# Kernel optimization log

Measured on AMD Instinct MI355X. Metric: run time of the kernel, lower is better.

The kernel has to match this reference:

```python
import jax, jax.numpy as jnp
import numpy as np

B, T, D = 64, 1024, 256   # batch, steps, obs dim
H, L, S = 512, 64, 4      # rnn hidden, latent dim, num_samples
LOG_2PI = float(np.log(2.0 * np.pi))


def setup_inputs() -> dict:
    key = jax.random.key(0)
    ks = jax.random.split(key, 6)
    return {
        "inputs": jax.random.normal(ks[0], (B, T, D), dtype=jnp.float32),
        "noise": jax.random.normal(ks[1], (T, S * B, L), dtype=jnp.float32),
        "W_x": jax.random.normal(ks[2], (D + L, 3 * H), dtype=jnp.float32) * 0.05,
        "W_h": jax.random.normal(ks[3], (H, 3 * H), dtype=jnp.float32) * 0.05,
        "b": jnp.zeros((3 * H,), dtype=jnp.float32),
        "W_d": jax.random.normal(ks[4], (H, 2 * L), dtype=jnp.float32) * 0.05,
        "b_d": jnp.zeros((2 * L,), dtype=jnp.float32),
    }


def _forward(inputs, noise, W_x, W_h, b, W_d, b_d):
    # inputs: [B, T, D]; scan over time with carry (rnn_state h, prev latent z)
    xs_t = jnp.swapaxes(inputs, 0, 1)  # [T, B, D]

    def step(carry, xs):
        h, z_prev = carry              # h: [S*B, H], z_prev: [S*B, L]
        x_t, eps_t = xs                # x_t: [B, D], eps_t: [S*B, L]
        x_tiled = jnp.tile(x_t, (S, 1))            # [S*B, D]
        rnn_in = jnp.concatenate([x_tiled, z_prev], axis=-1)  # [S*B, D+L]
        xg = rnn_in @ W_x + b                      # [S*B, 3H]
        hg_zr = h @ W_h[:, : 2 * H]                # update/reset recurrent part
        z_gate = jax.nn.sigmoid(xg[:, :H] + hg_zr[:, :H])
        r_gate = jax.nn.sigmoid(xg[:, H : 2 * H] + hg_zr[:, H:])
        n_cand = jnp.tanh(xg[:, 2 * H :] + (r_gate * h) @ W_h[:, 2 * H :])
        h_new = (1.0 - z_gate) * n_cand + z_gate * h  # GRU state, rnn_out == h_new
        # posterior dist p(z[t] | h[t]): diag Gaussian
        dp = h_new @ W_d + b_d                     # [S*B, 2L]
        mu, raw = dp[:, :L], dp[:, L:]
        sigma = jax.nn.softplus(raw) + 1e-4
        log_sigma = jnp.log(sigma)
        z = mu + sigma * eps_t                     # reparameterized sample
        ent = jnp.sum(0.5 * (LOG_2PI + 1.0) + log_sigma, axis=-1)          # [S*B]
        lp = jnp.sum(-0.5 * eps_t * eps_t - log_sigma - 0.5 * LOG_2PI, axis=-1)
        return (h_new, z), (z, ent, lp)

    h0 = jnp.zeros((S * B, H), dtype=inputs.dtype)
    z0 = jnp.zeros((S * B, L), dtype=inputs.dtype)
    _, (zs, ents, lps) = jax.lax.scan(step, (h0, z0), (xs_t, noise))
    # zs: [T, S*B, L] -> [S, B, T, L]
    sampled_z = jnp.swapaxes(zs, 0, 1).reshape(S, B, T, L)
    entropies = jnp.swapaxes(ents, 0, 1).reshape(S, B, T)
    log_probs = jnp.swapaxes(lps, 0, 1).reshape(S, B, T)
    return sampled_z, entropies, log_probs


def reference(inputs, noise, W_x, W_h, b, W_d, b_d):
    return _forward(inputs, noise, W_x, W_h, b, W_d, b_d)
```

## Files before the change

### kernel.cpp

```cpp
#include <hip/hip_runtime.h>
#include <stdint.h>


#define NWG  128u

typedef __bf16 bf16;
typedef __attribute__((ext_vector_type(8))) __bf16 bf16x8;
typedef __attribute__((ext_vector_type(8))) short  s16x8;
typedef __attribute__((ext_vector_type(4))) float  f32x4;
typedef __attribute__((ext_vector_type(4))) unsigned int u32x4;
typedef __attribute__((ext_vector_type(2))) unsigned long long u64x2;

__device__ __forceinline__ f32x4 mfma16(bf16x8 a, bf16x8 b, f32x4 c) {
  return __builtin_amdgcn_mfma_f32_16x16x32_bf16(
      __builtin_bit_cast(s16x8, a), __builtin_bit_cast(s16x8, b), c, 0, 0, 0);
}

__device__ __forceinline__ unsigned ld_u32_sc0(const unsigned* p) {
  unsigned v;
  asm volatile("global_load_dword %0, %1, off sc0\n\ts_waitcnt vmcnt(0)"
               : "=v"(v) : "v"(p) : "memory");
  return v;
}
__device__ __forceinline__ u32x4 ld_u128_sc0(const void* p) {
  u32x4 v;
  asm volatile("global_load_dwordx4 %0, %1, off sc0" : "=v"(v) : "v"(p));
  return v;
}
__device__ __forceinline__ void vm_wait0() {
  asm volatile("s_waitcnt vmcnt(0)" ::: "memory");
  __builtin_amdgcn_sched_barrier(0);
}

__global__ void repack_kernel(const float* __restrict__ W_x,
                              const float* __restrict__ W_h,
                              const float* __restrict__ W_d,
                              bf16* __restrict__ Whs, bf16* __restrict__ Wxz,
                              bf16* __restrict__ Wdf, bf16* __restrict__ Wxx)
{
  unsigned e = blockIdx.x*256u + threadIdx.x;
  if (e < 786432u) {
    unsigned c = e/49152u, r0 = e%49152u;
    unsigned kc = r0/3072u, r1 = r0%3072u;
    unsigned q = r1/768u, r2 = r1%768u;
    unsigned n = r2/8u, j = r2%8u;
    unsigned k = kc*32u + q*8u + j;
    unsigned colg = (n>>5)*512u + c*32u + (n&31u);
    Whs[e] = (bf16)W_h[k*1536u + colg];
  } else if (e < 884736u) {
    unsigned e1 = e - 786432u;
    unsigned c = e1/6144u, r0 = e1%6144u;
    unsigned kc = r0/3072u, r1 = r0%3072u;
    unsigned q = r1/768u, r2 = r1%768u;
    unsigned n = r2/8u, j = r2%8u;
    unsigned k = 256u + kc*32u + q*8u + j;
    unsigned colg = (n>>5)*512u + c*32u + (n&31u);
    Wxz[e1] = (bf16)W_x[k*1536u + colg];
  } else if (e < 950272u) {
    unsigned e2 = e - 884736u;
    unsigned kc = e2/4096u, r0 = e2%4096u;
    unsigned q = r0/1024u, r1 = r0%1024u;
    unsigned n = r1/8u, j = r1%8u;
    unsigned k = kc*32u + q*8u + j;
    Wdf[e2] = (bf16)W_d[k*128u + n];
  } else if (e < 1343488u) {
    unsigned e3 = e - 950272u;
    unsigned c = e3/24576u, r0 = e3%24576u;
    unsigned kc = r0/3072u, r1 = r0%3072u;
    unsigned q = r1/768u, r2 = r1%768u;
    unsigned n = r2/8u, j = r2%8u;
    unsigned k = kc*32u + q*8u + j;
    unsigned colg = (n>>5)*512u + c*32u + (n&31u);
    Wxx[e3] = (bf16)W_x[k*1536u + colg];
  }
}

__global__ void xpose_kernel(const float* __restrict__ x, bf16* __restrict__ xT)
{
  unsigned t = blockIdx.x, tid = threadIdx.x;
  unsigned row = tid>>2, seg = tid&3u;
  const float* src = x + ((size_t)row*1024u + t)*256u + seg*64u;
  bf16* dst = xT + (size_t)t*16384u + row*256u + seg*64u;
  #pragma unroll
  for (int i = 0; i < 8; ++i) {
    f32x4 v0 = *(const f32x4*)(src + i*8);
    f32x4 v1 = *(const f32x4*)(src + i*8 + 4);
    bf16x8 o;
    #pragma unroll
    for (int j = 0; j < 4; ++j) { o[j] = (bf16)v0[j]; o[4+j] = (bf16)v1[j]; }
    *(bf16x8*)(dst + i*8) = o;
  }
}

__global__ void __launch_bounds__(256) xgx_kernel(const bf16* __restrict__ xT,
                                                  const bf16* __restrict__ Wxx,
                                                  const float* __restrict__ bias,
                                                  bf16* __restrict__ xgx,
                                                  unsigned t0)
{
  __shared__ bf16 WxS[24576];
  __shared__ bf16 otile[6144];
  unsigned bid = blockIdx.x, lt = bid>>4, c = bid&15u, tid = threadIdx.x;
  unsigned t = t0 + lt;
  { const u32x4* s = (const u32x4*)(Wxx + (size_t)c*24576u); u32x4* d = (u32x4*)WxS;
    #pragma unroll
    for (int i=0;i<12;i++) d[tid+256u*i] = s[tid+256u*i]; }
  __syncthreads();
  unsigned wave = tid>>6, lane = tid&63u, q = lane>>4, m = lane&15u;
  f32x4 zero4 = {0.f,0.f,0.f,0.f};
  f32x4 acc[6];
  #pragma unroll
  for (int nt=0;nt<6;nt++) acc[nt] = zero4;
  const bf16* ap = xT + (size_t)t*16384u + (16u*wave + m)*256u + q*8u;
  #pragma unroll
  for (int kc=0;kc<8;kc++) {
    bf16x8 a = *(const bf16x8*)(ap + kc*32);
    #pragma unroll
    for (int nt=0;nt<6;nt++) {
      bf16x8 bb = *(const bf16x8*)(WxS + (((unsigned)kc*4u+q)*96u + (unsigned)nt*16u + m)*8u);
      acc[nt] = mfma16(a, bb, acc[nt]);
    }
  }
  #pragma unroll
  for (int nt=0;nt<6;nt++) {
    unsigned n = (unsigned)nt*16u + m;
    unsigned colg = (n>>5)*512u + c*32u + (n&31u);
    float bv = bias[colg];
    #pragma unroll
    for (int reg=0;reg<4;reg++)
      otile[(16u*wave + 4u*q + (unsigned)reg)*96u + n] = (bf16)(acc[nt][reg] + bv);
  }
  __syncthreads();
  { u32x4* d = (u32x4*)(xgx + (size_t)(lt*16u + c)*6144u);
    const u32x4* s = (const u32x4*)otile;
    #pragma unroll
    for (int i=0;i<3;i++) __builtin_nontemporal_store(s[tid+256u*i], d+tid+256u*i); }
}

__device__ __forceinline__ void rb_bar_llc(unsigned* __restrict__ flags,
                                           unsigned tid, unsigned lane,
                                           unsigned wave, unsigned c,
                                           unsigned target)
{
  __syncthreads();
  if (tid == 0)
    __hip_atomic_store(&flags[c], target, __ATOMIC_RELAXED,
                       __HIP_MEMORY_SCOPE_AGENT);
  if (wave == 0) {
    for (;;) {
      unsigned v = target;
      if (lane < 16u)
        v = __hip_atomic_load(&flags[lane], __ATOMIC_RELAXED,
                              __HIP_MEMORY_SCOPE_AGENT);
      if (__all((int)(v >= target))) break;
      __builtin_amdgcn_s_sleep(1);
    }
  }
  __syncthreads();
}
__device__ __forceinline__ void rb_bar_l2(unsigned* __restrict__ flags,
                                          unsigned tid, unsigned lane,
                                          unsigned c, unsigned target)
{
  __syncthreads();
  if (tid == 0)
    (void)__hip_atomic_exchange(&flags[c], target, __ATOMIC_RELAXED,
                                __HIP_MEMORY_SCOPE_WORKGROUP);
  for (;;) {
    unsigned v = target;
    if (lane < 16u) v = ld_u32_sc0(&flags[lane]);
    if (__all((int)(v >= target))) break;
  }
}

#define LDS_REC 159744
__global__ void __launch_bounds__(256, 1) rec_kernel(
    const bf16* __restrict__ Whs_g, const bf16* __restrict__ Wxz_g,
    const bf16* __restrict__ Wdf_g, const bf16* __restrict__ xgx,
    const float* __restrict__ noise, const float* __restrict__ b_d,
    float* __restrict__ out, bf16* __restrict__ hbuf, bf16* __restrict__ ubuf,
    bf16* __restrict__ zbuf, unsigned* __restrict__ bar,
    unsigned t0, unsigned tlen)
{
  extern __shared__ char smem[];
  bf16*  WhS  = (bf16*)(smem);
  bf16*  WxzS = (bf16*)(smem + 98304);
  bf16*  hA   = (bf16*)(smem + 110592);
  bf16*  zA   = (bf16*)(smem + 143360);
  bf16*  stg  = (bf16*)(smem + 147456);
  float* zgSf = (float*)(smem + 149504);
  bf16*  muS  = (bf16*)(smem + 147456);
  float* rawS = (float*)(smem + 151552);

  const unsigned tid = threadIdx.x;
  const unsigned wave = tid>>6, lane = tid&63u, q = lane>>4, m = lane&15u;
  const unsigned mt = wave&1u, gt = wave>>1;
  const unsigned r = blockIdx.x & 7u, c = blockIdx.x >> 3;
  const unsigned b0 = (r&1u)*32u;
  const unsigned rowG0 = r*32u;
  const unsigned zrow = tid>>3, zi = tid&7u;
  unsigned* rb = bar + (size_t)r*512u;

  { const u32x4* s = (const u32x4*)(Whs_g + (size_t)c*49152u); u32x4* d = (u32x4*)WhS;
    #pragma unroll
    for (int i=0;i<24;i++) d[tid+256u*i] = s[tid+256u*i]; }
  { const u32x4* s = (const u32x4*)(Wxz_g + (size_t)c*6144u); u32x4* d = (u32x4*)WxzS;
    #pragma unroll
    for (int i=0;i<3;i++) d[tid+256u*i] = s[tid+256u*i]; }
  bf16x8 wd[16][2];
  #pragma unroll
  for (int kc=0;kc<16;kc++) {
    #pragma unroll
    for (int nw=0;nw<2;nw++)
      wd[kc][nw] = *(const bf16x8*)(Wdf_g +
          ((((unsigned)kc*4u+q)*128u + wave*32u + (unsigned)nw*16u + m)*8u));
  }
  float bd0 = b_d[wave*32u + m], bd1 = b_d[wave*32u + 16u + m];

  bool l2m;
  {
    unsigned* ts = rb + 128u;
    unsigned myxcd;
    asm volatile("s_getreg_b32 %0, hwreg(HW_REG_XCC_ID)" : "=s"(myxcd));
    myxcd = (myxcd & 15u) + 1u;
    if (tid == 0)
      __hip_atomic_store(&rb[32u + c], myxcd, __ATOMIC_RELAXED,
                         __HIP_MEMORY_SCOPE_AGENT);
    rb_bar_llc(rb, tid, lane, wave, c, 1u);
    bool xcdok;
    { unsigned v = myxcd;
      if (lane < 16u)
        v = __hip_atomic_load(&rb[32u + lane], __ATOMIC_RELAXED,
                              __HIP_MEMORY_SCOPE_AGENT);
      xcdok = (bool)__all((int)(v == myxcd));
    }
    if (tid < 16u)
      __hip_atomic_store(&ts[c*16u + tid], 0xA0000000u + (c<<8) + tid,
                         __ATOMIC_RELAXED, __HIP_MEMORY_SCOPE_WORKGROUP);
    rb_bar_llc(rb, tid, lane, wave, c, 2u);
    unsigned jj = tid>>4, ii = tid&15u;
    bool okA = (ld_u32_sc0(&ts[tid]) == 0xA0000000u + (jj<<8) + ii);
    rb_bar_llc(rb, tid, lane, wave, c, 3u);
    if (tid < 16u)
      __hip_atomic_store(&ts[c*16u + tid], 0xB0000000u + (c<<8) + tid,
                         __ATOMIC_RELAXED, __HIP_MEMORY_SCOPE_WORKGROUP);
    rb_bar_llc(rb, tid, lane, wave, c, 4u);
    bool okB = (ld_u32_sc0(&ts[tid]) == 0xB0000000u + (jj<<8) + ii);
    unsigned* sc = (unsigned*)stg;
    sc[0] = 1u; __syncthreads();
    if (!(okA && okB)) sc[0] = 0u;
    __syncthreads();
    unsigned myok = (sc[0] != 0u) ? 1u : 2u;
    __syncthreads();
    if (tid == 0)
      __hip_atomic_store(&rb[96u + c], myok, __ATOMIC_RELAXED,
                         __HIP_MEMORY_SCOPE_AGENT);
    rb_bar_llc(rb, tid, lane, wave, c, 5u);
    { unsigned v = 1u;
      if (lane < 16u)
        v = __hip_atomic_load(&rb[96u + lane], __ATOMIC_RELAXED,
                              __HIP_MEMORY_SCOPE_AGENT);
      l2m = xcdok && (bool)__all((int)(v == 1u));
    }
  }
  unsigned* l2f = rb + 64u;

  float hstate[4];
  if (t0 == 0) {
    u32x4 zz = {0,0,0,0};
    u32x4* d = (u32x4*)hA;
    #pragma unroll
    for (int i=0;i<8;i++) d[tid+256u*i] = zz;
    ((u32x4*)zA)[tid] = zz;
    #pragma unroll
    for (int reg=0;reg<4;reg++) hstate[reg] = 0.f;
    __syncthreads();
  } else {
    const u32x4* s = (const u32x4*)(hbuf + ((size_t)(1u*8u + r)*16u)*1024u);
    u32x4* d = (u32x4*)hA;
    #pragma unroll
    for (int i=0;i<8;i++) d[tid+256u*i] = s[tid+256u*i];
    bf16x8 zv = *(const bf16x8*)(zbuf + ((size_t)(rowG0 + zrow)*64u + zi*8u));
    *(bf16x8*)(zA + ((size_t)zi*32u + zrow)*8u) = zv;
    __syncthreads();
    unsigned cl = gt*16u + m;
    #pragma unroll
    for (int reg=0;reg<4;reg++)
      hstate[reg] = (float)hA[((c*4u + (cl>>3))*32u + 16u*mt + 4u*q + (unsigned)reg)*8u + (cl&7u)];
  }

  const unsigned tend = t0 + tlen;
  for (unsigned t = t0; t < tend; ++t) {
    unsigned par = t & 1u;
    unsigned kb = 2u*(t - t0);
    __bf16 xv1[2][4]; __bf16 xv2[4];
    { size_t base = ((size_t)((t - t0)*16u + c)*64u + b0 + 16u*mt + 4u*q)*96u + m;
      #pragma unroll
      for (int nt=0;nt<2;nt++)
        #pragma unroll
        for (int reg=0;reg<4;reg++)
          xv1[nt][reg] = __builtin_nontemporal_load(
              &xgx[base + (unsigned)reg*96u + gt*32u + (unsigned)nt*16u]);
      #pragma unroll
      for (int reg=0;reg<4;reg++)
        xv2[reg] = __builtin_nontemporal_load(
            &xgx[base + (unsigned)reg*96u + 64u + gt*16u]);
    }
    f32x4 eps0, eps1;
    { const f32x4* np4 = (const f32x4*)(noise + ((size_t)t*256u + rowG0 + zrow)*64u + zi*8u);
      eps0 = __builtin_nontemporal_load(np4);
      eps1 = __builtin_nontemporal_load(np4 + 1); }

    f32x4 accP0 = {0.f,0.f,0.f,0.f}, accP1 = {0.f,0.f,0.f,0.f};
    #pragma unroll
    for (int kc=0;kc<2;kc++) {
      bf16x8 a = *(const bf16x8*)(zA + (((unsigned)kc*4u+q)*32u + 16u*mt + m)*8u);
      accP0 = mfma16(a, *(const bf16x8*)(WxzS + (((unsigned)kc*4u+q)*96u + gt*32u + m)*8u), accP0);
      accP1 = mfma16(a, *(const bf16x8*)(WxzS + (((unsigned)kc*4u+q)*96u + gt*32u + 16u + m)*8u), accP1);
    }
    #pragma unroll
    for (int kc=0;kc<16;kc++) {
      bf16x8 a = *(const bf16x8*)(hA + (((unsigned)kc*4u+q)*32u + 16u*mt + m)*8u);
      accP0 = mfma16(a, *(const bf16x8*)(WhS + (((unsigned)kc*4u+q)*96u + gt*32u + m)*8u), accP0);
      accP1 = mfma16(a, *(const bf16x8*)(WhS + (((unsigned)kc*4u+q)*96u + gt*32u + 16u + m)*8u), accP1);
    }
    #pragma unroll
    for (int reg=0;reg<4;reg++) {
      unsigned rloc = 16u*mt + 4u*q + (unsigned)reg;
      float g0 = accP0[reg] + (float)xv1[0][reg];
      float g1 = accP1[reg] + (float)xv1[1][reg];
      float s0 = 1.f/(1.f + __expf(-g0));
      float s1 = 1.f/(1.f + __expf(-g1));
      if (gt == 0) {
        zgSf[rloc*32u + m]       = s0;
        zgSf[rloc*32u + 16u + m] = s1;
      } else {
        unsigned cl0 = m, cl1 = 16u + m;
        float h0 = (float)hA[((c*4u + (cl0>>3))*32u + rloc)*8u + (cl0&7u)];
        float h1 = (float)hA[((c*4u + (cl1>>3))*32u + rloc)*8u + (cl1&7u)];
        stg[((cl0>>3)*32u + rloc)*8u + (cl0&7u)] = (bf16)(s0*h0);
        stg[((cl1>>3)*32u + rloc)*8u + (cl1&7u)] = (bf16)(s1*h1);
      }
    }
    __syncthreads();
    { size_t blk = ((size_t)(par*8u + r)*16u + c)*1024u;
      unsigned long long v = *(const unsigned long long*)(stg + (size_t)tid*4u);
      if (l2m)
        __hip_atomic_store((unsigned long long*)(ubuf + blk + (size_t)tid*4u), v,
                           __ATOMIC_RELAXED, __HIP_MEMORY_SCOPE_WORKGROUP);
      else
        __hip_atomic_store((unsigned long long*)(ubuf + blk + (size_t)tid*4u), v,
                           __ATOMIC_RELAXED, __HIP_MEMORY_SCOPE_AGENT); }
    if (l2m) rb_bar_l2 (l2f, tid, lane, c, kb + 1u);
    else     rb_bar_llc(rb,  tid, lane, wave, c, kb + 6u);

    bf16x8 ufr[16];
    if (l2m) {
      const char* ub = (const char*)ubuf + (size_t)(par*8u + r)*32768u
                       + (q*32u + 16u*mt + m)*16u;
      u32x4 tmp[16];
      #pragma unroll
      for (int kc=0;kc<16;kc++) tmp[kc] = ld_u128_sc0(ub + kc*2048);
      vm_wait0();
      #pragma unroll
      for (int kc=0;kc<16;kc++) ufr[kc] = __builtin_bit_cast(bf16x8, tmp[kc]);
    } else {
      unsigned long long* ubp = (unsigned long long*)ubuf;
      size_t b64 = ((size_t)(par*8u + r)*16u)*256u + (q*32u + 16u*mt + m)*2u;
      #pragma unroll
      for (int kc=0;kc<16;kc++) {
        unsigned long long a0 = __hip_atomic_load(ubp + b64 + (unsigned)kc*256u,
                                    __ATOMIC_RELAXED, __HIP_MEMORY_SCOPE_AGENT);
        unsigned long long a1 = __hip_atomic_load(ubp + b64 + (unsigned)kc*256u + 1u,
                                    __ATOMIC_RELAXED, __HIP_MEMORY_SCOPE_AGENT);
        u64x2 tt; tt[0] = a0; tt[1] = a1;
        ufr[kc] = __builtin_bit_cast(bf16x8, tt);
      }
    }
    f32x4 accNa = {0.f,0.f,0.f,0.f}, accNb = {0.f,0.f,0.f,0.f};
    #pragma unroll
    for (int kc=0;kc<2;kc++) {
      bf16x8 a = *(const bf16x8*)(zA + (((unsigned)kc*4u+q)*32u + 16u*mt + m)*8u);
      accNa = mfma16(a, *(const bf16x8*)(WxzS + (((unsigned)kc*4u+q)*96u + 64u + gt*16u + m)*8u), accNa);
    }
    #pragma unroll
    for (int kc=0;kc<16;kc++) {
      f32x4& acc = (kc & 1) ? accNb : accNa;
      acc = mfma16(ufr[kc], *(const bf16x8*)(WhS + (((unsigned)kc*4u+q)*96u + 64u + gt*16u + m)*8u), acc);
    }
    { unsigned colL2 = gt*16u + m;
      #pragma unroll
      for (int reg=0;reg<4;reg++) {
        unsigned rloc = 16u*mt + 4u*q + (unsigned)reg;
        float zg = zgSf[rloc*32u + colL2];
        float pre = accNa[reg] + accNb[reg] + (float)xv2[reg];
        float e2 = __expf(2.f*pre);
        float nc = 1.f - 2.f/(e2 + 1.f);
        float hn = (1.f - zg)*nc + zg*hstate[reg];
        hstate[reg] = hn;
        stg[((colL2>>3)*32u + rloc)*8u + (colL2&7u)] = (bf16)hn;
      }
    }
    __syncthreads();
    { size_t blk = ((size_t)(par*8u + r)*16u + c)*1024u;
      unsigned long long v = *(const unsigned long long*)(stg + (size_t)tid*4u);
      if (l2m)
        __hip_atomic_store((unsigned long long*)(hbuf + blk + (size_t)tid*4u), v,
                           __ATOMIC_RELAXED, __HIP_MEMORY_SCOPE_WORKGROUP);
      else
        __hip_atomic_store((unsigned long long*)(hbuf + blk + (size_t)tid*4u), v,
                           __ATOMIC_RELAXED, __HIP_MEMORY_SCOPE_AGENT); }
    if (l2m) rb_bar_l2 (l2f, tid, lane, c, kb + 2u);
    else     rb_bar_llc(rb,  tid, lane, wave, c, kb + 7u);
    if (l2m) {
      const char* hb = (const char*)hbuf + (size_t)(par*8u + r)*32768u
                       + (size_t)tid*16u;
      u32x4 g[8];
      #pragma unroll
      for (int i=0;i<8;i++) g[i] = ld_u128_sc0(hb + i*4096);
      vm_wait0();
      #pragma unroll
      for (int i=0;i<8;i++) ((u32x4*)hA)[tid + 256u*i] = g[i];
    } else {
      unsigned long long* s = (unsigned long long*)(hbuf + ((size_t)(par*8u + r)*16u)*1024u);
      unsigned long long* d = (unsigned long long*)hA;
      unsigned long long gtmp[16];
      #pragma unroll
      for (int i=0;i<16;i++)
        gtmp[i] = __hip_atomic_load(s + tid + 256u*i,
                                    __ATOMIC_RELAXED, __HIP_MEMORY_SCOPE_AGENT);
      #pragma unroll
      for (int i=0;i<16;i++) d[tid + 256u*i] = gtmp[i];
    }
    __syncthreads();

    f32x4 dp00={0.f,0.f,0.f,0.f}, dp01={0.f,0.f,0.f,0.f};
    f32x4 dp10={0.f,0.f,0.f,0.f}, dp11={0.f,0.f,0.f,0.f};
    #pragma unroll
    for (int kc=0;kc<16;kc++) {
      bf16x8 a0 = *(const bf16x8*)(hA + (((unsigned)kc*4u+q)*32u + m)*8u);
      bf16x8 a1 = *(const bf16x8*)(hA + (((unsigned)kc*4u+q)*32u + 16u + m)*8u);
      dp00 = mfma16(a0, wd[kc][0], dp00);
      dp01 = mfma16(a0, wd[kc][1], dp01);
      dp10 = mfma16(a1, wd[kc][0], dp10);
      dp11 = mfma16(a1, wd[kc][1], dp11);
    }
    if (wave < 2u) {
      #pragma unroll
      for (int reg=0;reg<4;reg++) {
        unsigned r0 = 4u*q + (unsigned)reg;
        muS[r0*64u + wave*32u + m]              = (bf16)(dp00[reg] + bd0);
        muS[r0*64u + wave*32u + 16u + m]        = (bf16)(dp01[reg] + bd1);
        muS[(r0+16u)*64u + wave*32u + m]        = (bf16)(dp10[reg] + bd0);
        muS[(r0+16u)*64u + wave*32u + 16u + m]  = (bf16)(dp11[reg] + bd1);
      }
    } else {
      unsigned cb = (wave - 2u)*32u;
      #pragma unroll
      for (int reg=0;reg<4;reg++) {
        unsigned r0 = 4u*q + (unsigned)reg;
        rawS[r0*64u + cb + m]              = dp00[reg] + bd0;
        rawS[r0*64u + cb + 16u + m]        = dp01[reg] + bd1;
        rawS[(r0+16u)*64u + cb + m]        = dp10[reg] + bd0;
        rawS[(r0+16u)*64u + cb + 16u + m]  = dp11[reg] + bd1;
      }
    }
    __syncthreads();
    {
      bf16x8 mu8 = *(const bf16x8*)(muS + (size_t)zrow*64u + zi*8u);
      f32x4 rw0 = *(const f32x4*)(rawS + (size_t)zrow*64u + zi*8u);
      f32x4 rw1 = *(const f32x4*)(rawS + (size_t)zrow*64u + zi*8u + 4u);
      float ent = 0.f, lp = 0.f;
      float zf[8];
      #pragma unroll
      for (int j=0;j<8;j++) {
        float raw = (j < 4) ? rw0[j] : rw1[j-4];
        float sp = (raw > 20.f) ? raw : __logf(1.f + __expf(raw));
        sp += 1e-4f;
        float ls = __logf(sp);
        float e = (j < 4) ? eps0[j] : eps1[j-4];
        float zv = (float)mu8[j] + sp*e;
        zf[j] = zv;
        ent += ls;
        lp  -= 0.5f*e*e + ls;
      }
      ent += 8.f*1.4189385332046727f;
      lp  -= 8.f*0.9189385332046727f;
      bf16x8 zb;
      #pragma unroll
      for (int j=0;j<8;j++) zb[j] = (bf16)zf[j];
      *(bf16x8*)(zA + ((size_t)zi*32u + zrow)*8u) = zb;
      if ((zrow>>1) == c) {
        float* zo = out + ((size_t)(rowG0 + zrow)*1024u + t)*64u + zi*8u;
        f32x4 o0 = {zf[0],zf[1],zf[2],zf[3]}, o1 = {zf[4],zf[5],zf[6],zf[7]};
        __builtin_nontemporal_store(o0, (f32x4*)zo);
        __builtin_nontemporal_store(o1, (f32x4*)zo + 1);
        if (t == tend - 1u)
          *(bf16x8*)(zbuf + ((size_t)(rowG0 + zrow)*64u + zi*8u)) = zb;
      }
      ent += __shfl_down(ent, 4); lp += __shfl_down(lp, 4);
      ent += __shfl_down(ent, 2); lp += __shfl_down(lp, 2);
      ent += __shfl_down(ent, 1); lp += __shfl_down(lp, 1);
      if (zi == 0u && (zrow>>1) == c) {
        __builtin_nontemporal_store(ent, &out[16777216u + (size_t)(rowG0 + zrow)*1024u + t]);
        __builtin_nontemporal_store(lp,  &out[17039360u + (size_t)(rowG0 + zrow)*1024u + t]);
      }
    }
    __syncthreads();
  }
}

extern "C" void kernel_launch(void* const* d_in, const int* in_sizes, int n_in,
                              void* d_out, int out_size, void* d_ws, size_t ws_size,
                              hipStream_t stream)
{
  const float* x     = (const float*)d_in[0];
  const float* noise = (const float*)d_in[1];
  const float* W_x   = (const float*)d_in[2];
  const float* W_h   = (const float*)d_in[3];
  const float* bias  = (const float*)d_in[4];
  const float* W_d   = (const float*)d_in[5];
  const float* b_d   = (const float*)d_in[6];
  float* out = (float*)d_out;
  char* ws = (char*)d_ws;

  size_t off = 0;
  unsigned* bar = (unsigned*)(ws + off);  off += 262144;
  bf16* Wdf  = (bf16*)(ws + off);         off += 65536ull*2;
  bf16* Whs  = (bf16*)(ws + off);         off += 786432ull*2;
  bf16* Wxz  = (bf16*)(ws + off);         off += 98304ull*2;
  bf16* Wxx  = (bf16*)(ws + off);         off += 393216ull*2;
  bf16* hbuf = (bf16*)(ws + off);         off += 262144ull*2;
  bf16* ubuf = (bf16*)(ws + off);         off += 262144ull*2;
  bf16* zbuf = (bf16*)(ws + off);         off += 16384ull*2;
  bf16* xT   = (bf16*)(ws + off);         off += 16777216ull*2;
  bf16* xgx  = (bf16*)(ws + off);
  size_t fixed = off;

  unsigned tlen = 1024;
  while (tlen > 64 && fixed + (size_t)tlen*196608ull > ws_size) tlen >>= 1;
  unsigned nch = 1024/tlen;

  hipMemsetAsync(bar, 0, 262144, stream);
  repack_kernel<<<5248, 256, 0, stream>>>(W_x, W_h, W_d, Whs, Wxz, Wdf, Wxx);
  xpose_kernel<<<1024, 256, 0, stream>>>(x, xT);
  hipFuncSetAttribute((const void*)rec_kernel,
                      hipFuncAttributeMaxDynamicSharedMemorySize, LDS_REC);
  for (unsigned ch = 0; ch < nch; ++ch) {
    unsigned t0 = ch*tlen;
    xgx_kernel<<<tlen*16, 256, 0, stream>>>(xT, Wxx, bias, xgx, t0);
    rec_kernel<<<NWG, 256, LDS_REC, stream>>>(Whs, Wxz, Wdf, xgx, noise, b_d,
                                              out, hbuf, ubuf, zbuf,
                                              bar + (size_t)ch*4096u, t0, tlen);
  }
}
```

Before: 8.979 ms.

## Streamline inter-workgroup barriers and prefetch next-step gate inputs and noise

Replaces the per-step cross-workgroup barrier with a lighter version. It uses raw s_barrier instead of __syncthreads, polls from a single wave, and pads the L2 flags onto separate 128-byte lines. The ubuf/hbuf publish stores become atomic exchanges, apparently to get an acknowledgement. Next-step xgx and noise are now loaded early, overlapping the recurrent matmul instead of sitting on the critical path, and the nontemporal hints on xgx are dropped so it stays cached. The raw barriers without a full fence carry memory-ordering risk, and prefetching adds register pressure.

Result: no change. 8.909 ms (-0.8%).

```diff
diff --git a/kernel.cpp b/kernel.cpp
--- a/kernel.cpp
+++ b/kernel.cpp
@@ -30,6 +30,19 @@
 __device__ __forceinline__ void vm_wait0() {
   asm volatile("s_waitcnt vmcnt(0)" ::: "memory");
   __builtin_amdgcn_sched_barrier(0);
+}
+__device__ __forceinline__ void bar_lds() {
+  asm volatile("s_waitcnt lgkmcnt(0)" ::: "memory");
+  __builtin_amdgcn_s_barrier();
+}
+__device__ __forceinline__ void st_ack(unsigned long long* p,
+                                       unsigned long long v, bool l2m) {
+  unsigned long long old;
+  if (l2m) old = __hip_atomic_exchange(p, v, __ATOMIC_RELAXED,
+                                       __HIP_MEMORY_SCOPE_WORKGROUP);
+  else     old = __hip_atomic_exchange(p, v, __ATOMIC_RELAXED,
+                                       __HIP_MEMORY_SCOPE_AGENT);
+  asm volatile("" :: "v"(old));
 }
 
 __global__ void repack_kernel(const float* __restrict__ W_x,
@@ -134,7 +147,7 @@
   { u32x4* d = (u32x4*)(xgx + (size_t)(lt*16u + c)*6144u);
     const u32x4* s = (const u32x4*)otile;
     #pragma unroll
-    for (int i=0;i<3;i++) __builtin_nontemporal_store(s[tid+256u*i], d+tid+256u*i); }
+    for (int i=0;i<3;i++) d[tid+256u*i] = s[tid+256u*i]; }
 }
 
 __device__ __forceinline__ void rb_bar_llc(unsigned* __restrict__ flags,
@@ -158,19 +171,40 @@
   }
   __syncthreads();
 }
-__device__ __forceinline__ void rb_bar_l2(unsigned* __restrict__ flags,
-                                          unsigned tid, unsigned lane,
-                                          unsigned c, unsigned target)
-{
-  __syncthreads();
-  if (tid == 0)
-    (void)__hip_atomic_exchange(&flags[c], target, __ATOMIC_RELAXED,
-                                __HIP_MEMORY_SCOPE_WORKGROUP);
-  for (;;) {
-    unsigned v = target;
-    if (lane < 16u) v = ld_u32_sc0(&flags[lane]);
-    if (__all((int)(v >= target))) break;
-  }
+
+__device__ __forceinline__ void xbar(unsigned* __restrict__ fl2,
+                                     unsigned* __restrict__ fllc, bool l2m,
+                                     unsigned tid, unsigned lane, unsigned wave,
+                                     unsigned c, unsigned tl2, unsigned tllc)
+{
+  __builtin_amdgcn_s_barrier();
+  if (l2m) {
+    if (tid == 0)
+      __hip_atomic_store(&fl2[c*32u], tl2, __ATOMIC_RELAXED,
+                         __HIP_MEMORY_SCOPE_WORKGROUP);
+    if (wave == 0) {
+      for (;;) {
+        unsigned v = tl2;
+        if (lane < 16u) v = ld_u32_sc0(&fl2[lane*32u]);
+        if (__all((int)(v >= tl2))) break;
+      }
+    }
+  } else {
+    if (tid == 0)
+      __hip_atomic_store(&fllc[c], tllc, __ATOMIC_RELAXED,
+                         __HIP_MEMORY_SCOPE_AGENT);
+    if (wave == 0) {
+      for (;;) {
+        unsigned v = tllc;
+        if (lane < 16u)
+          v = __hip_atomic_load(&fllc[lane], __ATOMIC_RELAXED,
+                                __HIP_MEMORY_SCOPE_AGENT);
+        if (__all((int)(v >= tllc))) break;
+        __builtin_amdgcn_s_sleep(1);
+      }
+    }
+  }
+  __builtin_amdgcn_s_barrier();
 }
 
 #define LDS_REC 159744
@@ -199,7 +233,8 @@
   const unsigned b0 = (r&1u)*32u;
   const unsigned rowG0 = r*32u;
   const unsigned zrow = tid>>3, zi = tid&7u;
-  unsigned* rb = bar + (size_t)r*512u;
+  unsigned* rb  = bar + (size_t)r*1024u;
+  unsigned* l2f = rb + 512u;
 
   { const u32x4* s = (const u32x4*)(Whs_g + (size_t)c*49152u); u32x4* d = (u32x4*)WhS;
     #pragma unroll
@@ -263,7 +298,6 @@
       l2m = xcdok && (bool)__all((int)(v == 1u));
     }
   }
-  unsigned* l2f = rb + 64u;
 
   float hstate[4];
   if (t0 == 0) {
@@ -290,26 +324,23 @@
   }
 
   const unsigned tend = t0 + tlen;
+  __bf16 xc1[2][4]; __bf16 xc2[4]; f32x4 ec0, ec1;
+  { size_t base = ((size_t)(0u*16u + c)*64u + b0 + 16u*mt + 4u*q)*96u + m;
+    #pragma unroll
+    for (int nt=0;nt<2;nt++)
+      #pragma unroll
+      for (int reg=0;reg<4;reg++)
+        xc1[nt][reg] = xgx[base + (unsigned)reg*96u + gt*32u + (unsigned)nt*16u];
+    #pragma unroll
+    for (int reg=0;reg<4;reg++)
+      xc2[reg] = xgx[base + (unsigned)reg*96u + 64u + gt*16u];
+    const f32x4* np4 = (const f32x4*)(noise + ((size_t)t0*256u + rowG0 + zrow)*64u + zi*8u);
+    ec0 = np4[0]; ec1 = np4[1];
+  }
+
   for (unsigned t = t0; t < tend; ++t) {
     unsigned par = t & 1u;
     unsigned kb = 2u*(t - t0);
-    __bf16 xv1[2][4]; __bf16 xv2[4];
-    { size_t base = ((size_t)((t - t0)*16u + c)*64u + b0 + 16u*mt + 4u*q)*96u + m;
-      #pragma unroll
-      for (int nt=0;nt<2;nt++)
-        #pragma unroll
-        for (int reg=0;reg<4;reg++)
-          xv1[nt][reg] = __builtin_nontemporal_load(
-              &xgx[base + (unsigned)reg*96u + gt*32u + (unsigned)nt*16u]);
-      #pragma unroll
-      for (int reg=0;reg<4;reg++)
-        xv2[reg] = __builtin_nontemporal_load(
-            &xgx[base + (unsigned)reg*96u + 64u + gt*16u]);
-    }
-    f32x4 eps0, eps1;
-    { const f32x4* np4 = (const f32x4*)(noise + ((size_t)t*256u + rowG0 + zrow)*64u + zi*8u);
-      eps0 = __builtin_nontemporal_load(np4);
-      eps1 = __builtin_nontemporal_load(np4 + 1); }
 
     f32x4 accP0 = {0.f,0.f,0.f,0.f}, accP1 = {0.f,0.f,0.f,0.f};
     #pragma unroll
@@ -327,8 +358,8 @@
     #pragma unroll
     for (int reg=0;reg<4;reg++) {
       unsigned rloc = 16u*mt + 4u*q + (unsigned)reg;
-      float g0 = accP0[reg] + (float)xv1[0][reg];
-      float g1 = accP1[reg] + (float)xv1[1][reg];
+      float g0 = accP0[reg] + (float)xc1[0][reg];
+      float g1 = accP1[reg] + (float)xc1[1][reg];
       float s0 = 1.f/(1.f + __expf(-g0));
       float s1 = 1.f/(1.f + __expf(-g1));
       if (gt == 0) {
@@ -342,17 +373,11 @@
         stg[((cl1>>3)*32u + rloc)*8u + (cl1&7u)] = (bf16)(s1*h1);
       }
     }
-    __syncthreads();
+    bar_lds();
     { size_t blk = ((size_t)(par*8u + r)*16u + c)*1024u;
       unsigned long long v = *(const unsigned long long*)(stg + (size_t)tid*4u);
-      if (l2m)
-        __hip_atomic_store((unsigned long long*)(ubuf + blk + (size_t)tid*4u), v,
-                           __ATOMIC_RELAXED, __HIP_MEMORY_SCOPE_WORKGROUP);
-      else
-        __hip_atomic_store((unsigned long long*)(ubuf + blk + (size_t)tid*4u), v,
-                           __ATOMIC_RELAXED, __HIP_MEMORY_SCOPE_AGENT); }
-    if (l2m) rb_bar_l2 (l2f, tid, lane, c, kb + 1u);
-    else     rb_bar_llc(rb,  tid, lane, wave, c, kb + 6u);
+      st_ack((unsigned long long*)(ubuf + blk + (size_t)tid*4u), v, l2m); }
+    xbar(l2f, rb, l2m, tid, lane, wave, c, kb + 1u, kb + 6u);
 
     bf16x8 ufr[16];
     if (l2m) {
@@ -377,6 +402,20 @@
         ufr[kc] = __builtin_bit_cast(bf16x8, tt);
       }
     }
+    __bf16 xn1[2][4]; __bf16 xn2[4]; f32x4 en0, en1;
+    { unsigned tn = (t + 1u < tend) ? (t + 1u) : t;
+      size_t base = ((size_t)((tn - t0)*16u + c)*64u + b0 + 16u*mt + 4u*q)*96u + m;
+      #pragma unroll
+      for (int nt=0;nt<2;nt++)
+        #pragma unroll
+        for (int reg=0;reg<4;reg++)
+          xn1[nt][reg] = xgx[base + (unsigned)reg*96u + gt*32u + (unsigned)nt*16u];
+      #pragma unroll
+      for (int reg=0;reg<4;reg++)
+        xn2[reg] = xgx[base + (unsigned)reg*96u + 64u + gt*16u];
+      const f32x4* np4 = (const f32x4*)(noise + ((size_t)tn*256u + rowG0 + zrow)*64u + zi*8u);
+      en0 = np4[0]; en1 = np4[1];
+    }
     f32x4 accNa = {0.f,0.f,0.f,0.f}, accNb = {0.f,0.f,0.f,0.f};
     #pragma unroll
     for (int kc=0;kc<2;kc++) {
@@ -393,7 +432,7 @@
       for (int reg=0;reg<4;reg++) {
         unsigned rloc = 16u*mt + 4u*q + (unsigned)reg;
         float zg = zgSf[rloc*32u + colL2];
-        float pre = accNa[reg] + accNb[reg] + (float)xv2[reg];
+        float pre = accNa[reg] + accNb[reg] + (float)xc2[reg];
         float e2 = __expf(2.f*pre);
         float nc = 1.f - 2.f/(e2 + 1.f);
         float hn = (1.f - zg)*nc + zg*hstate[reg];
@@ -401,17 +440,11 @@
         stg[((colL2>>3)*32u + rloc)*8u + (colL2&7u)] = (bf16)hn;
       }
     }
-    __syncthreads();
+    bar_lds();
     { size_t blk = ((size_t)(par*8u + r)*16u + c)*1024u;
       unsigned long long v = *(const unsigned long long*)(stg + (size_t)tid*4u);
-      if (l2m)
-        __hip_atomic_store((unsigned long long*)(hbuf + blk + (size_t)tid*4u), v,
-                           __ATOMIC_RELAXED, __HIP_MEMORY_SCOPE_WORKGROUP);
-      else
-        __hip_atomic_store((unsigned long long*)(hbuf + blk + (size_t)tid*4u), v,
-                           __ATOMIC_RELAXED, __HIP_MEMORY_SCOPE_AGENT); }
-    if (l2m) rb_bar_l2 (l2f, tid, lane, c, kb + 2u);
-    else     rb_bar_llc(rb,  tid, lane, wave, c, kb + 7u);
+      st_ack((unsigned long long*)(hbuf + blk + (size_t)tid*4u), v, l2m); }
+    xbar(l2f, rb, l2m, tid, lane, wave, c, kb + 2u, kb + 7u);
     if (l2m) {
       const char* hb = (const char*)hbuf + (size_t)(par*8u + r)*32768u
                        + (size_t)tid*16u;
@@ -432,7 +465,7 @@
       #pragma unroll
       for (int i=0;i<16;i++) d[tid + 256u*i] = gtmp[i];
     }
-    __syncthreads();
+    bar_lds();
 
     f32x4 dp00={0.f,0.f,0.f,0.f}, dp01={0.f,0.f,0.f,0.f};
     f32x4 dp10={0.f,0.f,0.f,0.f}, dp11={0.f,0.f,0.f,0.f};
@@ -465,7 +498,7 @@
         rawS[(r0+16u)*64u + cb + 16u + m]  = dp11[reg] + bd1;
       }
     }
-    __syncthreads();
+    bar_lds();
     {
       bf16x8 mu8 = *(const bf16x8*)(muS + (size_t)zrow*64u + zi*8u);
       f32x4 rw0 = *(const f32x4*)(rawS + (size_t)zrow*64u + zi*8u);
@@ -478,7 +511,7 @@
         float sp = (raw > 20.f) ? raw : __logf(1.f + __expf(raw));
         sp += 1e-4f;
         float ls = __logf(sp);
-        float e = (j < 4) ? eps0[j] : eps1[j-4];
+        float e = (j < 4) ? ec0[j] : ec1[j-4];
         float zv = (float)mu8[j] + sp*e;
         zf[j] = zv;
         ent += ls;
@@ -506,7 +539,14 @@
         __builtin_nontemporal_store(lp,  &out[17039360u + (size_t)(rowG0 + zrow)*1024u + t]);
       }
     }
-    __syncthreads();
+    bar_lds();
+    #pragma unroll
+    for (int nt=0;nt<2;nt++)
+      #pragma unroll
+      for (int reg=0;reg<4;reg++) xc1[nt][reg] = xn1[nt][reg];
+    #pragma unroll
+    for (int reg=0;reg<4;reg++) xc2[reg] = xn2[reg];
+    ec0 = en0; ec1 = en1;
   }
 }
 
@@ -525,7 +565,7 @@
   char* ws = (char*)d_ws;
 
   size_t off = 0;
-  unsigned* bar = (unsigned*)(ws + off);  off += 262144;
+  unsigned* bar = (unsigned*)(ws + off);  off += 524288;
   bf16* Wdf  = (bf16*)(ws + off);         off += 65536ull*2;
   bf16* Whs  = (bf16*)(ws + off);         off += 786432ull*2;
   bf16* Wxz  = (bf16*)(ws + off);         off += 98304ull*2;
@@ -541,7 +581,7 @@
   while (tlen > 64 && fixed + (size_t)tlen*196608ull > ws_size) tlen >>= 1;
   unsigned nch = 1024/tlen;
 
-  hipMemsetAsync(bar, 0, 262144, stream);
+  hipMemsetAsync(bar, 0, 524288, stream);
   repack_kernel<<<5248, 256, 0, stream>>>(W_x, W_h, W_d, Whs, Wxz, Wdf, Wxx);
   xpose_kernel<<<1024, 256, 0, stream>>>(x, xT);
   hipFuncSetAttribute((const void*)rec_kernel,
@@ -551,6 +591,6 @@
     xgx_kernel<<<tlen*16, 256, 0, stream>>>(xT, Wxx, bias, xgx, t0);
     rec_kernel<<<NWG, 256, LDS_REC, stream>>>(Whs, Wxz, Wdf, xgx, noise, b_d,
                                               out, hbuf, ubuf, zbuf,
-                                              bar + (size_t)ch*4096u, t0, tlen);
-  }
-}
+                                              bar + (size_t)ch*8192u, t0, tlen);
+  }
+}
```
